# Optimization experiments

Measured on AMD Instinct MI355X. Metric: run time of the kernel, lower is better.

Reference implementation:

```python
import jax, jax.numpy as jnp
import numpy as np

NEG_INF = -1e6  # d2l masked_softmax fill value


def setup_inputs() -> dict:
    key = jax.random.key(0)
    kq, kk, kv, kl = jax.random.split(key, 4)
    n, s, d = 32, 2048, 64
    queries = jax.random.normal(kq, (n, s, d), dtype=jnp.float32)
    keys = jax.random.normal(kk, (n, s, d), dtype=jnp.float32)
    values = jax.random.normal(kv, (n, s, d), dtype=jnp.float32)
    valid_lens = jax.random.randint(kl, (n,), 1, s + 1, dtype=jnp.int32)
    return {"queries": queries, "keys": keys, "values": values, "valid_lens": valid_lens}


def reference(queries, keys, values, valid_lens):
    d = queries.shape[-1]
    # scores: [n, q, k]
    scores = jnp.einsum("nqd,nkd->nqk", queries, keys) / jnp.sqrt(jnp.float32(d))
    kv_len = scores.shape[-1]
    # masked_softmax: positions >= valid_len get NEG_INF before softmax
    mask = jnp.arange(kv_len, dtype=jnp.int32)[None, None, :] < valid_lens[:, None, None]
    scores = jnp.where(mask, scores, NEG_INF)
    attn = jax.nn.softmax(scores, axis=-1)
    # dropout rate 0.0 (inference) -> identity
    return jnp.einsum("nqk,nkd->nqd", attn, values)
```

## Files before the change

kernel.cpp:

```cpp
#include <hip/hip_runtime.h>
#include <hip/hip_bf16.h>


typedef short bf16x8 __attribute__((ext_vector_type(8)));
typedef float f32x4  __attribute__((ext_vector_type(4)));
typedef float f32x16 __attribute__((ext_vector_type(16)));
typedef unsigned int u32;
typedef u32 u32x4 __attribute__((ext_vector_type(4)));

#define SEQ 2048
#define DH 64
#define BK 64
#define LDSP 72
#define FRAG 512
#define TILE_SH 4096
#define PSTRIDE 36
#define SCLQ 0.18033688011112042f

static __device__ __forceinline__ short f2bf(float f) {
    unsigned u = __float_as_uint(f);
    return (short)((u + 0x7FFFu + ((u >> 16) & 1u)) >> 16);
}
static __device__ __forceinline__ u32 pk2bf(float lo, float hi) {
    __hip_bfloat162 h = __float22bfloat162_rn(float2{lo, hi});
    return *(u32*)&h;
}
static __device__ __forceinline__ void pl32swap(u32& a, u32& b) {
    asm volatile("v_permlane32_swap_b32 %0, %1" : "+v"(a), "+v"(b));
}

__global__ __launch_bounds__(256, 4)
void prepass(const float* __restrict__ K, const float* __restrict__ V,
             short* __restrict__ KF, short* __restrict__ VF)
{
    __shared__ short T[DH][LDSP];

    const int tid  = threadIdx.x;
    const int wave = tid >> 6;
    const int lane = tid & 63;
    const int b  = blockIdx.x & 31;
    const int t  = blockIdx.x >> 5;
    const int k0 = t * BK;
    const size_t bo = (size_t)b * SEQ * DH;
    const size_t tb = (size_t)(b * 32 + t) * TILE_SH;

    const float* Ks = K + bo + (size_t)k0 * DH;
    short* Kd = KF + tb;
    #pragma unroll
    for (int h = 0; h < 2; ++h) {
        const int c = tid + h * 256;
        const int f = c >> 6;
        const int row = (f & 1) * 32 + (c & 31);
        const int col = (f >> 1) * 16 + ((c >> 5) & 1) * 8;
        f32x4 a = *(const f32x4*)(Ks + row * DH + col);
        f32x4 d = *(const f32x4*)(Ks + row * DH + col + 4);
        u32x4 o;
        o[0] = pk2bf(a[0], a[1]); o[1] = pk2bf(a[2], a[3]);
        o[2] = pk2bf(d[0], d[1]); o[3] = pk2bf(d[2], d[3]);
        *(u32x4*)(Kd + c * 8) = o;
    }

    #pragma unroll
    for (int h = 0; h < 2; ++h) {
        const int d0 = wave * 8 + h * 32;
        const float* src = V + bo + (size_t)(k0 + lane) * DH + d0;
        f32x4 va = *(const f32x4*)(src);
        f32x4 vb = *(const f32x4*)(src + 4);
        #pragma unroll
        for (int j = 0; j < 4; ++j) {
            T[d0 + j][lane]     = f2bf(va[j]);
            T[d0 + 4 + j][lane] = f2bf(vb[j]);
        }
    }
    __syncthreads();

    short* Vd = VF + tb;
    #pragma unroll
    for (int h = 0; h < 2; ++h) {
        const int c = tid + h * 256;
        const int f = c >> 6;
        const int trow = (f & 1) * 32 + (c & 31);
        const int tcol = (f >> 1) * 16 + ((c >> 5) & 1) * 8;
        *(bf16x8*)(Vd + c * 8) = *(const bf16x8*)(&T[trow][tcol]);
    }
}

template <bool PRE>
__global__ __launch_bounds__(256, 4)
void attn_fwd(const float* __restrict__ Q,
              const float* __restrict__ Kf, const float* __restrict__ Vf,
              const short* __restrict__ KF, const short* __restrict__ VF,
              const int* __restrict__ VL, float* __restrict__ O)
{
    __shared__ __align__(16) float Red[2][64][PSTRIDE];
    __shared__ int Rsort[32];

    const int tid  = threadIdx.x;
    const int wave = tid >> 6;
    const int lane = tid & 63;
    const int hi   = lane >> 5;
    const int l31  = lane & 31;

    if (tid < 32) {
        const int nv = (VL[tid] + BK - 1) >> 6;
        int rank = 0;
        for (int jj = 0; jj < 32; ++jj) {
            const int nj = (VL[jj] + BK - 1) >> 6;
            rank += (nj > nv) || (nj == nv && jj < tid);
        }
        Rsort[rank] = tid;
    }
    __syncthreads();

    const int qq = blockIdx.x & 63;
    const int rk = blockIdx.x >> 6;
    int b = Rsort[rk];
    b = __builtin_amdgcn_readfirstlane(b);

    const int vl  = __builtin_amdgcn_readfirstlane(VL[b]);
    const int nkt = (vl + BK - 1) >> 6;

    const size_t bo = (size_t)b * SEQ * DH;
    const short* KFb = KF + (size_t)b * 32 * TILE_SH;
    const short* VFb = VF + (size_t)b * 32 * TILE_SH;
    const float* Kf32 = Kf + bo;
    const float* Vf32 = Vf + bo;

    const int qrow = qq * 32 + l31;
    bf16x8 aq[4];
    {
        const float* qp = Q + bo + (size_t)qrow * DH + hi * 8;
        #pragma unroll
        for (int st = 0; st < 4; ++st) {
            f32x4 a = *(const f32x4*)(qp + st * 16);
            f32x4 c = *(const f32x4*)(qp + st * 16 + 4);
            #pragma unroll
            for (int j = 0; j < 4; ++j) {
                aq[st][j]     = f2bf(a[j] * SCLQ);
                aq[st][j + 4] = f2bf(c[j] * SCLQ);
            }
        }
    }

    f32x16 oacc0, oacc1;
    #pragma unroll
    for (int i = 0; i < 16; ++i) { oacc0[i] = 0.f; oacc1[i] = 0.f; }
    float Lrun = 0.f;

    const int lo8 = lane * 8;

    for (int kt = wave; kt < nkt; kt += 4) {
        const int k0 = kt * BK;
        const short* kf = KFb + (size_t)kt * TILE_SH;
        const short* vf = VFb + (size_t)kt * TILE_SH;

        auto ldA = [&](int f) -> bf16x8 {
            if constexpr (PRE) {
                return *(const bf16x8*)(kf + f * FRAG + lo8);
            } else {
                const int st = f >> 1, kh = f & 1;
                const float* p = Kf32 + (size_t)(k0 + kh * 32 + l31) * DH + st * 16 + hi * 8;
                f32x4 x = *(const f32x4*)p;
                f32x4 y = *(const f32x4*)(p + 4);
                bf16x8 rr;
                #pragma unroll
                for (int j = 0; j < 4; ++j) { rr[j] = f2bf(x[j]); rr[j + 4] = f2bf(y[j]); }
                return rr;
            }
        };
        auto ldV = [&](int f) -> bf16x8 {
            if constexpr (PRE) {
                return *(const bf16x8*)(vf + f * FRAG + lo8);
            } else {
                const int ks = f >> 1, dh = f & 1;
                bf16x8 rr;
                #pragma unroll
                for (int j = 0; j < 8; ++j)
                    rr[j] = f2bf(Vf32[(size_t)(k0 + ks * 16 + hi * 8 + j) * DH + dh * 32 + l31]);
                return rr;
            }
        };

        f32x16 s0, s1;
        #pragma unroll
        for (int i = 0; i < 16; ++i) { s0[i] = 0.f; s1[i] = 0.f; }

        __builtin_amdgcn_s_setprio(1);
        bf16x8 A00 = ldA(0), A01 = ldA(1);
        bf16x8 A10 = ldA(2), A11 = ldA(3);
        s0 = __builtin_amdgcn_mfma_f32_32x32x16_bf16(A00, aq[0], s0, 0, 0, 0);
        s1 = __builtin_amdgcn_mfma_f32_32x32x16_bf16(A01, aq[0], s1, 0, 0, 0);
        bf16x8 A20 = ldA(4), A21 = ldA(5);
        s0 = __builtin_amdgcn_mfma_f32_32x32x16_bf16(A10, aq[1], s0, 0, 0, 0);
        s1 = __builtin_amdgcn_mfma_f32_32x32x16_bf16(A11, aq[1], s1, 0, 0, 0);
        bf16x8 A30 = ldA(6), A31 = ldA(7);
        s0 = __builtin_amdgcn_mfma_f32_32x32x16_bf16(A20, aq[2], s0, 0, 0, 0);
        s1 = __builtin_amdgcn_mfma_f32_32x32x16_bf16(A21, aq[2], s1, 0, 0, 0);
        s0 = __builtin_amdgcn_mfma_f32_32x32x16_bf16(A30, aq[3], s0, 0, 0, 0);
        s1 = __builtin_amdgcn_mfma_f32_32x32x16_bf16(A31, aq[3], s1, 0, 0, 0);
        __builtin_amdgcn_s_setprio(0);

        bf16x8 V00 = ldV(0), V01 = ldV(1);
        bf16x8 V10 = ldV(2), V11 = ldV(3);

        if (k0 + BK <= vl) {
            #pragma unroll
            for (int r = 0; r < 16; ++r) {
                s0[r] = __builtin_amdgcn_exp2f(s0[r]);
                s1[r] = __builtin_amdgcn_exp2f(s1[r]);
            }
        } else {
            #pragma unroll
            for (int r = 0; r < 16; ++r) {
                const int krow = k0 + (r & 3) + 8 * (r >> 2) + 4 * hi;
                s0[r] = (krow < vl)      ? __builtin_amdgcn_exp2f(s0[r]) : 0.f;
                s1[r] = (krow + 32 < vl) ? __builtin_amdgcn_exp2f(s1[r]) : 0.f;
            }
        }

        {
            float ls = 0.f;
            #pragma unroll
            for (int r = 0; r < 16; ++r) ls += s0[r] + s1[r];
            u32 a = __float_as_uint(ls), c = a;
            pl32swap(a, c);
            Lrun += __uint_as_float(a) + __uint_as_float(c);
        }

        u32 pk0[8], pk1[8];
        #pragma unroll
        for (int i = 0; i < 8; ++i) {
            pk0[i] = pk2bf(s0[2 * i], s0[2 * i + 1]);
            pk1[i] = pk2bf(s1[2 * i], s1[2 * i + 1]);
        }
        bf16x8 ap[4];
        #pragma unroll
        for (int t = 0; t < 2; ++t) {
            u32 x0 = pk0[4 * t], x1 = pk0[4 * t + 1];
            u32 x2 = pk0[4 * t + 2], x3 = pk0[4 * t + 3];
            pl32swap(x0, x2); pl32swap(x1, x3);
            u32x4 w; w[0] = x0; w[1] = x1; w[2] = x2; w[3] = x3;
            ap[t] = *(bf16x8*)&w;
            u32 y0 = pk1[4 * t], y1 = pk1[4 * t + 1];
            u32 y2 = pk1[4 * t + 2], y3 = pk1[4 * t + 3];
            pl32swap(y0, y2); pl32swap(y1, y3);
            u32x4 v; v[0] = y0; v[1] = y1; v[2] = y2; v[3] = y3;
            ap[2 + t] = *(bf16x8*)&v;
        }

        __builtin_amdgcn_s_setprio(1);
        oacc0 = __builtin_amdgcn_mfma_f32_32x32x16_bf16(ap[0], V00, oacc0, 0, 0, 0);
        oacc1 = __builtin_amdgcn_mfma_f32_32x32x16_bf16(ap[0], V01, oacc1, 0, 0, 0);
        bf16x8 V20 = ldV(4), V21 = ldV(5);
        oacc0 = __builtin_amdgcn_mfma_f32_32x32x16_bf16(ap[1], V10, oacc0, 0, 0, 0);
        oacc1 = __builtin_amdgcn_mfma_f32_32x32x16_bf16(ap[1], V11, oacc1, 0, 0, 0);
        bf16x8 V30 = ldV(6), V31 = ldV(7);
        oacc0 = __builtin_amdgcn_mfma_f32_32x32x16_bf16(ap[2], V20, oacc0, 0, 0, 0);
        oacc1 = __builtin_amdgcn_mfma_f32_32x32x16_bf16(ap[2], V21, oacc1, 0, 0, 0);
        oacc0 = __builtin_amdgcn_mfma_f32_32x32x16_bf16(ap[3], V30, oacc0, 0, 0, 0);
        oacc1 = __builtin_amdgcn_mfma_f32_32x32x16_bf16(ap[3], V31, oacc1, 0, 0, 0);
        __builtin_amdgcn_s_setprio(0);
    }

    if (wave & 1) {
        float* rp = &Red[wave >> 1][lane][0];
        #pragma unroll
        for (int wd = 0; wd < 4; ++wd) {
            f32x4 t0, t1;
            #pragma unroll
            for (int i = 0; i < 4; ++i) { t0[i] = oacc0[wd * 4 + i]; t1[i] = oacc1[wd * 4 + i]; }
            *(f32x4*)(rp + wd * 4)      = t0;
            *(f32x4*)(rp + 16 + wd * 4) = t1;
        }
        rp[32] = Lrun;
    }
    __syncthreads();
    if (!(wave & 1)) {
        const float* rp = &Red[wave >> 1][lane][0];
        #pragma unroll
        for (int wd = 0; wd < 4; ++wd) {
            f32x4 t0 = *(const f32x4*)(rp + wd * 4);
            f32x4 t1 = *(const f32x4*)(rp + 16 + wd * 4);
            #pragma unroll
            for (int i = 0; i < 4; ++i) { oacc0[wd * 4 + i] += t0[i]; oacc1[wd * 4 + i] += t1[i]; }
        }
        Lrun += rp[32];
    }
    __syncthreads();
    if (wave == 2) {
        float* rp = &Red[0][lane][0];
        #pragma unroll
        for (int wd = 0; wd < 4; ++wd) {
            f32x4 t0, t1;
            #pragma unroll
            for (int i = 0; i < 4; ++i) { t0[i] = oacc0[wd * 4 + i]; t1[i] = oacc1[wd * 4 + i]; }
            *(f32x4*)(rp + wd * 4)      = t0;
            *(f32x4*)(rp + 16 + wd * 4) = t1;
        }
        rp[32] = Lrun;
    }
    __syncthreads();
    if (wave == 0) {
        const float* rp = &Red[0][lane][0];
        #pragma unroll
        for (int wd = 0; wd < 4; ++wd) {
            f32x4 t0 = *(const f32x4*)(rp + wd * 4);
            f32x4 t1 = *(const f32x4*)(rp + 16 + wd * 4);
            #pragma unroll
            for (int i = 0; i < 4; ++i) { oacc0[wd * 4 + i] += t0[i]; oacc1[wd * 4 + i] += t1[i]; }
        }
        const float Lq = Lrun + rp[32];
        #pragma unroll
        for (int r = 0; r < 16; ++r) {
            const int rb = (r & 3) + 8 * (r >> 2) + 4 * hi;
            const float inv = 1.0f / __shfl(Lq, rb);
            const int row = qq * 32 + rb;
            O[bo + (size_t)row * DH + l31]      = oacc0[r] * inv;
            O[bo + (size_t)row * DH + 32 + l31] = oacc1[r] * inv;
        }
    }
}

extern "C" void kernel_launch(void* const* d_in, const int* in_sizes, int n_in,
                              void* d_out, int out_size, void* d_ws, size_t ws_size,
                              hipStream_t stream) {
    const float* Q  = (const float*)d_in[0];
    const float* K  = (const float*)d_in[1];
    const float* V  = (const float*)d_in[2];
    const int*   VL = (const int*)d_in[3];
    float* O = (float*)d_out;

    const size_t nel  = (size_t)32 * 32 * TILE_SH;
    const size_t need = 2 * nel * sizeof(short);
    if (ws_size >= need) {
        short* KF = (short*)d_ws;
        short* VF = KF + nel;
        prepass<<<dim3(1024), dim3(256), 0, stream>>>(K, V, KF, VF);
        attn_fwd<true><<<dim3(2048), dim3(256), 0, stream>>>(Q, K, V, KF, VF, VL, O);
    } else {
        attn_fwd<false><<<dim3(2048), dim3(256), 0, stream>>>(Q, K, V, nullptr, nullptr, VL, O);
    }
}
```

Measured before the change: 129.9 us.

## Prefetch next K tile into registers and remap blocks across XCDs

The K fragments for the next tile a wave owns are now loaded into registers during the current iteration, right after the QK MFMAs, so global load latency overlaps the softmax and PV work. The block index is also remapped so that consecutive blocks, which the hardware spreads across the eight XCDs, take batches in a serpentine order over the sorted valid-length ranking. This is meant to balance the uneven per-batch work across XCDs and improve L2 locality. The prefetch costs 8 more bf16x8 registers per lane, which may reduce occupancy.

```diff
diff --git a/kernel.cpp b/kernel.cpp
--- a/kernel.cpp
+++ b/kernel.cpp
@@ -112,8 +112,12 @@
     }
     __syncthreads();
 
-    const int qq = blockIdx.x & 63;
-    const int rk = blockIdx.x >> 6;
+    const int xcd = blockIdx.x & 7;
+    const int w   = blockIdx.x >> 3;
+    const int sel = w >> 6;
+    const int qq  = w & 63;
+    const int rk  = (sel == 0) ? xcd : (sel == 1) ? (15 - xcd)
+                  : (sel == 2) ? (16 + xcd) : (31 - xcd);
     int b = Rsort[rk];
     b = __builtin_amdgcn_readfirstlane(b);
 
@@ -149,25 +153,28 @@
 
     const int lo8 = lane * 8;
 
+    bf16x8 Ac[8];
+    if (PRE && wave < nkt) {
+        const short* kf0 = KFb + (size_t)wave * TILE_SH;
+        #pragma unroll
+        for (int f = 0; f < 8; ++f) Ac[f] = *(const bf16x8*)(kf0 + f * FRAG + lo8);
+    }
+
     for (int kt = wave; kt < nkt; kt += 4) {
         const int k0 = kt * BK;
-        const short* kf = KFb + (size_t)kt * TILE_SH;
         const short* vf = VFb + (size_t)kt * TILE_SH;
 
-        auto ldA = [&](int f) -> bf16x8 {
-            if constexpr (PRE) {
-                return *(const bf16x8*)(kf + f * FRAG + lo8);
-            } else {
+        if constexpr (!PRE) {
+            #pragma unroll
+            for (int f = 0; f < 8; ++f) {
                 const int st = f >> 1, kh = f & 1;
                 const float* p = Kf32 + (size_t)(k0 + kh * 32 + l31) * DH + st * 16 + hi * 8;
                 f32x4 x = *(const f32x4*)p;
                 f32x4 y = *(const f32x4*)(p + 4);
-                bf16x8 rr;
                 #pragma unroll
-                for (int j = 0; j < 4; ++j) { rr[j] = f2bf(x[j]); rr[j + 4] = f2bf(y[j]); }
-                return rr;
-            }
-        };
+                for (int j = 0; j < 4; ++j) { Ac[f][j] = f2bf(x[j]); Ac[f][j + 4] = f2bf(y[j]); }
+            }
+        }
         auto ldV = [&](int f) -> bf16x8 {
             if constexpr (PRE) {
                 return *(const bf16x8*)(vf + f * FRAG + lo8);
@@ -186,19 +193,20 @@
         for (int i = 0; i < 16; ++i) { s0[i] = 0.f; s1[i] = 0.f; }
 
         __builtin_amdgcn_s_setprio(1);
-        bf16x8 A00 = ldA(0), A01 = ldA(1);
-        bf16x8 A10 = ldA(2), A11 = ldA(3);
-        s0 = __builtin_amdgcn_mfma_f32_32x32x16_bf16(A00, aq[0], s0, 0, 0, 0);
-        s1 = __builtin_amdgcn_mfma_f32_32x32x16_bf16(A01, aq[0], s1, 0, 0, 0);
-        bf16x8 A20 = ldA(4), A21 = ldA(5);
-        s0 = __builtin_amdgcn_mfma_f32_32x32x16_bf16(A10, aq[1], s0, 0, 0, 0);
-        s1 = __builtin_amdgcn_mfma_f32_32x32x16_bf16(A11, aq[1], s1, 0, 0, 0);
-        bf16x8 A30 = ldA(6), A31 = ldA(7);
-        s0 = __builtin_amdgcn_mfma_f32_32x32x16_bf16(A20, aq[2], s0, 0, 0, 0);
-        s1 = __builtin_amdgcn_mfma_f32_32x32x16_bf16(A21, aq[2], s1, 0, 0, 0);
-        s0 = __builtin_amdgcn_mfma_f32_32x32x16_bf16(A30, aq[3], s0, 0, 0, 0);
-        s1 = __builtin_amdgcn_mfma_f32_32x32x16_bf16(A31, aq[3], s1, 0, 0, 0);
+        #pragma unroll
+        for (int st = 0; st < 4; ++st) {
+            s0 = __builtin_amdgcn_mfma_f32_32x32x16_bf16(Ac[2 * st],     aq[st], s0, 0, 0, 0);
+            s1 = __builtin_amdgcn_mfma_f32_32x32x16_bf16(Ac[2 * st + 1], aq[st], s1, 0, 0, 0);
+        }
         __builtin_amdgcn_s_setprio(0);
+
+        bf16x8 An[8];
+        const bool pf = PRE && (kt + 4 < nkt);
+        if (pf) {
+            const short* kfn = KFb + (size_t)(kt + 4) * TILE_SH;
+            #pragma unroll
+            for (int f = 0; f < 8; ++f) An[f] = *(const bf16x8*)(kfn + f * FRAG + lo8);
+        }
 
         bf16x8 V00 = ldV(0), V01 = ldV(1);
         bf16x8 V10 = ldV(2), V11 = ldV(3);
@@ -239,13 +247,13 @@
             u32 x0 = pk0[4 * t], x1 = pk0[4 * t + 1];
             u32 x2 = pk0[4 * t + 2], x3 = pk0[4 * t + 3];
             pl32swap(x0, x2); pl32swap(x1, x3);
-            u32x4 w; w[0] = x0; w[1] = x1; w[2] = x2; w[3] = x3;
-            ap[t] = *(bf16x8*)&w;
+            u32x4 w4; w4[0] = x0; w4[1] = x1; w4[2] = x2; w4[3] = x3;
+            ap[t] = *(bf16x8*)&w4;
             u32 y0 = pk1[4 * t], y1 = pk1[4 * t + 1];
             u32 y2 = pk1[4 * t + 2], y3 = pk1[4 * t + 3];
             pl32swap(y0, y2); pl32swap(y1, y3);
-            u32x4 v; v[0] = y0; v[1] = y1; v[2] = y2; v[3] = y3;
-            ap[2 + t] = *(bf16x8*)&v;
+            u32x4 v4; v4[0] = y0; v4[1] = y1; v4[2] = y2; v4[3] = y3;
+            ap[2 + t] = *(bf16x8*)&v4;
         }
 
         __builtin_amdgcn_s_setprio(1);
@@ -260,6 +268,11 @@
         oacc0 = __builtin_amdgcn_mfma_f32_32x32x16_bf16(ap[3], V30, oacc0, 0, 0, 0);
         oacc1 = __builtin_amdgcn_mfma_f32_32x32x16_bf16(ap[3], V31, oacc1, 0, 0, 0);
         __builtin_amdgcn_s_setprio(0);
+
+        if (pf) {
+            #pragma unroll
+            for (int f = 0; f < 8; ++f) Ac[f] = An[f];
+        }
     }
 
     if (wave & 1) {
```

Measured after the change: 171.2 us. 1.32x slower.
